# Kernel optimization log

Hardware: AMD Instinct MI355X
Metric: run time of the kernel (lower is better)

## Reference

```python
import jax, jax.numpy as jnp
import numpy as np

N_QUBITS = 15
N_LAYERS = 1
DIM = 2 ** N_QUBITS
N_PQC = 4 * N_QUBITS * N_LAYERS
CDTYPE = jnp.complex64


def _apply_1q(state, U, w):
    # state: (2,)*N tensor; apply 2x2 U on axis w
    s = jnp.tensordot(U, state, axes=((1,), (w,)))
    return jnp.moveaxis(s, 0, w)


def _ry_mat(theta):
    c = jnp.cos(theta / 2).astype(CDTYPE)
    s = jnp.sin(theta / 2).astype(CDTYPE)
    return jnp.stack([jnp.stack([c, -s]), jnp.stack([s, c])])


def _rx_mat(theta):
    c = jnp.cos(theta / 2).astype(CDTYPE)
    s = (-1j * jnp.sin(theta / 2)).astype(CDTYPE)
    return jnp.stack([jnp.stack([c, s]), jnp.stack([s, c])])


def _apply_crx(state, theta, ctrl, tgt):
    # controlled-RX: apply RX to target slice where control qubit = 1
    s0 = jax.lax.index_in_dim(state, 0, axis=ctrl, keepdims=False)
    s1 = jax.lax.index_in_dim(state, 1, axis=ctrl, keepdims=False)
    t = tgt if tgt < ctrl else tgt - 1
    s1 = _apply_1q(s1, _rx_mat(theta), t)
    return jnp.stack([s0, s1], axis=ctrl)


def _evolve(params, state):
    # ansatz 14 (Sim et al. 2019); params: [4*N_QUBITS*N_LAYERS]
    n = N_QUBITS
    idx = 0
    for _ in range(N_LAYERS):
        for i in range(n):
            state = _apply_1q(state, _ry_mat(params[idx]), i); idx += 1
        for i in range(n - 1, -1, -1):
            state = _apply_crx(state, params[idx], i, (i + 1) % n); idx += 1
        for i in range(n):
            state = _apply_1q(state, _ry_mat(params[idx]), i); idx += 1
        for i in [n - 1] + list(range(n - 1)):
            state = _apply_crx(state, params[idx], i, (i - 1) % n); idx += 1
    return state


def _measure_xyz(state):
    # expval of PauliX, PauliY, PauliZ on each wire -> [3*N_QUBITS] real
    xs, ys, zs = [], [], []
    for w in range(N_QUBITS):
        a = jnp.moveaxis(state, w, 0).reshape(2, -1)
        z01 = jnp.conj(a[0]) * a[1]
        xs.append(2.0 * jnp.sum(z01.real))
        ys.append(2.0 * jnp.sum(z01.imag))
        zs.append(jnp.sum(jnp.abs(a[0]) ** 2 - jnp.abs(a[1]) ** 2))
    return jnp.stack(xs + ys + zs)


def _forward(tokens_emb, W, b, qsvt_coeffs, lcu_coeffs_ri, ff_params):
    angles = tokens_emb @ W.T + b  # [L, N_PQC]
    lcu = lcu_coeffs_ri[:, 0] + 1j * lcu_coeffs_ri[:, 1]
    lcu = (lcu / jnp.maximum(jnp.sum(jnp.abs(lcu)), 1e-8)).astype(CDTYPE)
    e0 = jnp.zeros((DIM,), CDTYPE).at[0].set(1.0)

    def apply_lcu(mono):
        norm = jnp.linalg.norm(mono)
        small = norm < 1e-8
        safe = jnp.where(small, 1.0, norm)
        init = jnp.where(small, e0, mono / safe).reshape((2,) * N_QUBITS)
        evolved = jax.vmap(lambda p: _evolve(p, init).reshape(-1))(angles)  # [L, DIM]
        out = jnp.einsum('td,t->d', evolved, lcu)
        return jnp.where(small, 1.0, norm) * out

    acc = qsvt_coeffs[0] * e0
    mono = e0
    for k in range(1, qsvt_coeffs.shape[0]):
        mono = apply_lcu(mono)
        acc = acc + qsvt_coeffs[k] * mono
    acc = acc / jnp.maximum(jnp.sum(jnp.abs(qsvt_coeffs)), 1e-8)
    snorm = jnp.linalg.norm(acc)
    small = snorm < 1e-8
    safe = jnp.where(small, 1.0, snorm)
    ff_in = jnp.where(small, e0, acc / safe).reshape((2,) * N_QUBITS)
    final = _evolve(ff_params, ff_in)
    return _measure_xyz(final)


def setup_inputs() -> dict:
    key = jax.random.key(0)
    ks = jax.random.split(key, 6)
    d_model, n_tokens = 1024, 32
    tokens_emb = jax.random.normal(ks[0], (n_tokens, d_model), jnp.float32)
    W = jax.random.normal(ks[1], (N_PQC, d_model), jnp.float32) / np.float32(np.sqrt(d_model))
    b = jax.random.normal(ks[2], (N_PQC,), jnp.float32) * 0.01
    qsvt_coeffs = jax.random.normal(ks[3], (4,), jnp.float32) * 0.1
    lcu_coeffs_ri = jax.random.normal(ks[4], (n_tokens, 2), jnp.float32)
    ff_params = jax.random.normal(ks[5], (N_PQC,), jnp.float32)
    return {"tokens_emb": tokens_emb, "W": W, "b": b, "qsvt_coeffs": qsvt_coeffs,
            "lcu_coeffs_ri": lcu_coeffs_ri, "ff_params": ff_params}


def reference(tokens_emb, W, b, qsvt_coeffs, lcu_coeffs_ri, ff_params):
    return _forward(tokens_emb, W, b, qsvt_coeffs, lcu_coeffs_ri, ff_params)
```

## Files before the change

kernel.cpp:

```cpp
#include <hip/hip_runtime.h>

#define NQ    15
#define DIM   32768
#define NTOK  32
#define NPQC  60
#define TPB   512
#define KREG  64
#define CHUNK 16

template<int... Is> struct iseq {};
template<int N, int... Is> struct mkseq : mkseq<N-1, N-1, Is...> {};
template<int... Is> struct mkseq<0, Is...> { using type = iseq<Is...>; };

__device__ __forceinline__ float wsum(float v){
  #pragma unroll
  for (int m = 1; m < 64; m <<= 1) v += __shfl_xor(v, m, 64);
  return v;
}


template<int CPOS>
__device__ __forceinline__ bool cbit(int r, int tid, int blk){
  if constexpr (CPOS < 0)        return true;
  else if constexpr (CPOS == 0)  return (r & 1) != 0;
  else if constexpr (CPOS == 10) return (r & 2) != 0;
  else if constexpr (CPOS == 11) return (r & 4) != 0;
  else if constexpr (CPOS <= 9)  return ((tid >> (CPOS - 1)) & 1) != 0;
  else                           return ((blk >> (CPOS - 12)) & 1) != 0;
}

template<int TPOS, int CPOS, bool RX>
__device__ __forceinline__ void gate_rl(float2 cs, float (&vr)[8], float (&vi)[8], int tid, int blk){
  constexpr int tm = (TPOS == 0) ? 1 : (TPOS == 10 ? 2 : 4);
  const float c = cs.x, s = cs.y;
  #pragma unroll
  for (int r0 = 0; r0 < 8; ++r0){
    if (r0 & tm) continue;
    const int r1 = r0 | tm;
    const bool act = cbit<CPOS>(r0, tid, blk);
    const float ar = vr[r0], ai = vi[r0], br = vr[r1], bi = vi[r1];
    if (act){
      if constexpr (RX){
        vr[r0] = fmaf(c, ar,  s * bi); vi[r0] = fmaf(c, ai, -s * br);
        vr[r1] = fmaf(c, br,  s * ai); vi[r1] = fmaf(c, bi, -s * ar);
      } else {
        vr[r0] = fmaf(c, ar, -s * br); vi[r0] = fmaf(c, ai, -s * bi);
        vr[r1] = fmaf(c, br,  s * ar); vi[r1] = fmaf(c, bi,  s * ai);
      }
    }
  }
}

template<int TPOS, int CPOS, bool RX>
__device__ __forceinline__ void gate_ln(float2 cs, float (&vr)[8], float (&vi)[8], int tid, int blk){
  constexpr int bm = 1 << (TPOS - 1);
  const float c = cs.x, s = cs.y;
  const int side = (tid >> (TPOS - 1)) & 1;
  const float sg = side ? s : -s;
  #pragma unroll
  for (int r = 0; r < 8; ++r){
    const float pr = __shfl_xor(vr[r], bm, 64);
    const float pi = __shfl_xor(vi[r], bm, 64);
    const bool act = cbit<CPOS>(r, tid, blk);
    float nr, ni;
    if constexpr (RX){ nr = fmaf(c, vr[r],  s * pi); ni = fmaf(c, vi[r], -s * pr); }
    else             { nr = fmaf(c, vr[r], sg * pr); ni = fmaf(c, vi[r], sg * pi); }
    if (act){ vr[r] = nr; vi[r] = ni; }
  }
}

template<int TPOS, int CPOS, bool RX>
__device__ __forceinline__ void gate_wv(float2 cs, float (&vr)[8], float (&vi)[8], int tid, int blk, float2* ex){
  constexpr int tb = TPOS - 1;
  const int ptid = tid ^ (1 << tb);
  const float c = cs.x, s = cs.y;
  const int side = (tid >> tb) & 1;
  const float sg = side ? s : -s;
  __syncthreads();
  #pragma unroll
  for (int r = 0; r < 8; ++r) ex[(r << 9) | tid] = make_float2(vr[r], vi[r]);
  __syncthreads();
  #pragma unroll
  for (int r = 0; r < 8; ++r){
    const float2 p = ex[(r << 9) | ptid];
    const bool act = cbit<CPOS>(r, tid, blk);
    float nr, ni;
    if constexpr (RX){ nr = fmaf(c, vr[r],  s * p.y); ni = fmaf(c, vi[r], -s * p.x); }
    else             { nr = fmaf(c, vr[r], sg * p.x); ni = fmaf(c, vi[r], sg * p.y); }
    if (act){ vr[r] = nr; vi[r] = ni; }
  }
}

template<int TPOS, int CPOS, bool RX>
__device__ __forceinline__ void G(float2 cs, float (&vr)[8], float (&vi)[8], int tid, int blk, float2* ex){
  if constexpr (TPOS == 0 || TPOS == 10 || TPOS == 11) gate_rl<TPOS,CPOS,RX>(cs, vr, vi, tid, blk);
  else if constexpr (TPOS <= 6)                        gate_ln<TPOS,CPOS,RX>(cs, vr, vi, tid, blk);
  else                                                 gate_wv<TPOS,CPOS,RX>(cs, vr, vi, tid, blk, ex);
}

#define SEG_LOAD(SRC)                                                        \
  {                                                                          \
    const int t2 = tid << 1;                                                 \
    _Pragma("unroll")                                                        \
    for (int rh = 0; rh < 4; ++rh){                                          \
      const int r2 = rh >> 1, r1 = rh & 1, ra = (r1 << 1) | (r2 << 2);       \
      const float4 v = *reinterpret_cast<const float4*>(&(SRC)[(r2 << 11) + (r1 << 10) + t2]); \
      vr[ra] = v.x; vi[ra] = v.y; vr[ra + 1] = v.z; vi[ra + 1] = v.w;        \
    }                                                                        \
  }

__global__ __launch_bounds__(512) void seg1_k(const float2* __restrict__ in, float2* __restrict__ out,
    const float2* __restrict__ cs, int csStride, const float* __restrict__ parts, int np,
    int finalMode, const float* __restrict__ qsvt)
{
  __shared__ float2 ex[4096];
  __shared__ float2 gcs[12];
  const int tid = threadIdx.x, blk = blockIdx.x, tok = blockIdx.y;
  if (tid < 12) gcs[tid] = cs[tok * csStride + tid];
  bool small = false; float inv = 1.f;
  if (np > 0){
    const int lane = tid & 63;
    float p = lane < np ? parts[lane] : 0.f;
    const float nv = sqrtf(wsum(p));
    if (finalMode){
      const float qs = fmaxf(fabsf(qsvt[0]) + fabsf(qsvt[1]) + fabsf(qsvt[2]) + fabsf(qsvt[3]), 1e-8f);
      small = (nv / qs) < 1e-8f;
    } else small = nv < 1e-8f;
    inv = small ? 0.f : 1.f / nv;
  }
  float vr[8], vi[8];
  const float2* src = in + (blk << 12);
  {
    const int t2 = tid << 1;
    #pragma unroll
    for (int rh = 0; rh < 4; ++rh){
      const int r2 = rh >> 1, r1 = rh & 1, ra = (r1 << 1) | (r2 << 2);
      const float4 v = *reinterpret_cast<const float4*>(&src[(r2 << 11) + (r1 << 10) + t2]);
      vr[ra] = v.x * inv; vi[ra] = v.y * inv; vr[ra + 1] = v.z * inv; vi[ra + 1] = v.w * inv;
    }
  }
  if (small){
    #pragma unroll
    for (int r = 0; r < 8; ++r){ vr[r] = (blk == 0 && tid == 0 && r == 0) ? 1.f : 0.f; vi[r] = 0.f; }
  }
  __syncthreads();
  G<11,-1,false>(gcs[0], vr, vi, tid, blk, ex);
  G<10,-1,false>(gcs[1], vr, vi, tid, blk, ex);
  G< 9,-1,false>(gcs[2], vr, vi, tid, blk, ex);
  G< 8,-1,false>(gcs[3], vr, vi, tid, blk, ex);
  G< 7,-1,false>(gcs[4], vr, vi, tid, blk, ex);
  G< 6,-1,false>(gcs[5], vr, vi, tid, blk, ex);
  G< 5,-1,false>(gcs[6], vr, vi, tid, blk, ex);
  G< 4,-1,false>(gcs[7], vr, vi, tid, blk, ex);
  G< 3,-1,false>(gcs[8], vr, vi, tid, blk, ex);
  G< 2,-1,false>(gcs[9], vr, vi, tid, blk, ex);
  G< 1,-1,false>(gcs[10], vr, vi, tid, blk, ex);
  G< 0,-1,false>(gcs[11], vr, vi, tid, blk, ex);
  float2* dst = out + ((size_t)tok << 15);
  const int bb = ((blk & 1) << 5) | ((blk & 2) << 5) | ((blk & 4) << 8);
  const int tb = ((tid & 15) << 1) | ((tid & 112) << 3) | ((tid & 384) << 5);
  #pragma unroll
  for (int r1 = 0; r1 < 2; ++r1)
    #pragma unroll
    for (int r0 = 0; r0 < 2; ++r0){
      const int r = r0 | (r1 << 1);
      const int a = bb + tb + (r0 << 11) + (r1 << 14);
      *reinterpret_cast<float4*>(&dst[a]) = make_float4(vr[r], vi[r], vr[r + 4], vi[r + 4]);
    }
}

__global__ __launch_bounds__(512) void seg2_k(const float2* __restrict__ in, float2* __restrict__ out,
    const float2* __restrict__ cs, int csStride)
{
  __shared__ float2 ex[4096];
  __shared__ float2 gcs[15];
  const int tid = threadIdx.x, blk = blockIdx.x, tok = blockIdx.y;
  if (tid < 15) gcs[tid] = cs[tok * csStride + 12 + tid];
  float vr[8], vi[8];
  const float2* src = in + ((size_t)tok << 15) + (blk << 12);
  SEG_LOAD(src);
  __syncthreads();
  G<10,-1,false>(gcs[0], vr, vi, tid, blk, ex);
  G< 6,-1,false>(gcs[1], vr, vi, tid, blk, ex);
  G< 5,-1,false>(gcs[2], vr, vi, tid, blk, ex);
  G< 0, 5,true >(gcs[3], vr, vi, tid, blk, ex);
  G< 5, 6,true >(gcs[4], vr, vi, tid, blk, ex);
  G< 6,10,true >(gcs[5], vr, vi, tid, blk, ex);
  G<10,11,true >(gcs[6], vr, vi, tid, blk, ex);
  G<11, 1,true >(gcs[7], vr, vi, tid, blk, ex);
  G< 1, 2,true >(gcs[8], vr, vi, tid, blk, ex);
  G< 2, 3,true >(gcs[9], vr, vi, tid, blk, ex);
  G< 3, 4,true >(gcs[10], vr, vi, tid, blk, ex);
  G< 4, 7,true >(gcs[11], vr, vi, tid, blk, ex);
  G< 7, 8,true >(gcs[12], vr, vi, tid, blk, ex);
  G< 8, 9,true >(gcs[13], vr, vi, tid, blk, ex);
  G< 9,12,true >(gcs[14], vr, vi, tid, blk, ex);
  float2* dst = out + ((size_t)tok << 15);
  const int bb = ((blk & 1) << 11) | ((blk & 2) << 5) | ((blk & 4) << 3);
  const int tb = ((tid & 7) << 1) | ((tid & 8) << 7) | ((tid & 16) << 8) | ((tid & 32) << 8) | ((tid & 448) << 1);
  #pragma unroll
  for (int r1 = 0; r1 < 2; ++r1)
    #pragma unroll
    for (int r0 = 0; r0 < 2; ++r0){
      const int r = r0 | (r1 << 1);
      const int a = bb + tb + (r0 << 4) + (r1 << 14);
      *reinterpret_cast<float4*>(&dst[a]) = make_float4(vr[r], vi[r], vr[r + 4], vi[r + 4]);
    }
}

__global__ __launch_bounds__(512) void seg3_k(const float2* __restrict__ in, float2* __restrict__ out,
    const float2* __restrict__ cs, int csStride)
{
  __shared__ float2 ex[4096];
  __shared__ float2 gcs[15];
  const int tid = threadIdx.x, blk = blockIdx.x, tok = blockIdx.y;
  if (tid < 15) gcs[tid] = cs[tok * csStride + 27 + tid];
  float vr[8], vi[8];
  const float2* src = in + ((size_t)tok << 15) + (blk << 12);
  SEG_LOAD(src);
  __syncthreads();
  G<11, 6,true >(gcs[0], vr, vi, tid, blk, ex);
  G< 6, 5,true >(gcs[1], vr, vi, tid, blk, ex);
  G< 5, 4,true >(gcs[2], vr, vi, tid, blk, ex);
  G< 4,-1,false>(gcs[3], vr, vi, tid, blk, ex);
  G< 5,-1,false>(gcs[4], vr, vi, tid, blk, ex);
  G< 6,-1,false>(gcs[5], vr, vi, tid, blk, ex);
  G<11,-1,false>(gcs[6], vr, vi, tid, blk, ex);
  G< 9,-1,false>(gcs[7], vr, vi, tid, blk, ex);
  G< 8,-1,false>(gcs[8], vr, vi, tid, blk, ex);
  G< 7,-1,false>(gcs[9], vr, vi, tid, blk, ex);
  G<10,-1,false>(gcs[10], vr, vi, tid, blk, ex);
  G< 3,-1,false>(gcs[11], vr, vi, tid, blk, ex);
  G< 2,-1,false>(gcs[12], vr, vi, tid, blk, ex);
  G< 1,-1,false>(gcs[13], vr, vi, tid, blk, ex);
  G< 0,-1,false>(gcs[14], vr, vi, tid, blk, ex);
  float2* dst = out + ((size_t)tok << 15);
  const int bb = ((blk & 1) << 5) | ((blk & 2) << 5) | ((blk & 4) << 8);
  const int tb = ((tid & 1) << 13) | ((tid & 2) << 13) | ((tid & 60) >> 1) | ((tid & 448) << 1);
  #pragma unroll
  for (int r2 = 0; r2 < 2; ++r2)
    #pragma unroll
    for (int r0 = 0; r0 < 2; ++r0){
      const int r = r0 | (r2 << 2);
      const int a = bb + tb + (r0 << 12) + (r2 << 11);
      *reinterpret_cast<float4*>(&dst[a]) = make_float4(vr[r], vi[r], vr[r + 2], vi[r + 2]);
    }
}

__global__ __launch_bounds__(512) void seg4_k(const float2* __restrict__ in, float2* __restrict__ out,
    const float2* __restrict__ cs, int csStride)
{
  __shared__ float2 ex[4096];
  __shared__ float2 gcs[14];
  const int tid = threadIdx.x, blk = blockIdx.x, tok = blockIdx.y;
  if (tid < 14) gcs[tid] = cs[tok * csStride + 42 + tid];
  float vr[8], vi[8];
  const float2* src = in + ((size_t)tok << 15) + (blk << 12);
  SEG_LOAD(src);
  __syncthreads();
  G<10,-1,false>(gcs[0], vr, vi, tid, blk, ex);
  G< 6,-1,false>(gcs[1], vr, vi, tid, blk, ex);
  G< 5,-1,false>(gcs[2], vr, vi, tid, blk, ex);
  G< 6, 5,true >(gcs[3], vr, vi, tid, blk, ex);
  G< 5, 2,true >(gcs[4], vr, vi, tid, blk, ex);
  G< 2, 3,true >(gcs[5], vr, vi, tid, blk, ex);
  G< 3, 4,true >(gcs[6], vr, vi, tid, blk, ex);
  G< 4,11,true >(gcs[7], vr, vi, tid, blk, ex);
  G<11, 9,true >(gcs[8], vr, vi, tid, blk, ex);
  G< 9, 8,true >(gcs[9], vr, vi, tid, blk, ex);
  G< 8, 7,true >(gcs[10], vr, vi, tid, blk, ex);
  G< 7, 0,true >(gcs[11], vr, vi, tid, blk, ex);
  G< 0, 1,true >(gcs[12], vr, vi, tid, blk, ex);
  G< 1,14,true >(gcs[13], vr, vi, tid, blk, ex);
  float2* dst = out + ((size_t)tok << 15);
  const int bb = ((blk & 1) << 10) | ((blk & 2) << 2) | ((blk & 4) << 2);
  const int tb = ((tid & 1) << 5) | ((tid & 2) << 13) | ((tid & 4) << 11) | ((tid & 8) << 9)
               | ((tid & 48) >> 3) | ((tid & 448) << 1);
  #pragma unroll
  for (int r2 = 0; r2 < 2; ++r2)
    #pragma unroll
    for (int r0 = 0; r0 < 2; ++r0){
      const int r = r0 | (r2 << 2);
      const int a = bb + tb + (r0 << 6) + (r2 << 11);
      *reinterpret_cast<float4*>(&dst[a]) = make_float4(vr[r], vi[r], vr[r + 2], vi[r + 2]);
    }
}

__global__ __launch_bounds__(512) void seg5_k(const float2* __restrict__ in, float2* __restrict__ out,
    const float2* __restrict__ cs, int csStride)
{
  __shared__ float2 ex[4096];
  __shared__ float2 gcs[4];
  const int tid = threadIdx.x, blk = blockIdx.x, tok = blockIdx.y;
  if (tid < 4) gcs[tid] = cs[tok * csStride + 56 + tid];
  float vr[8], vi[8];
  const float2* src = in + ((size_t)tok << 15) + (blk << 12);
  SEG_LOAD(src);
  __syncthreads();
  G< 4, 3,true >(gcs[0], vr, vi, tid, blk, ex);
  G< 3,10,true >(gcs[1], vr, vi, tid, blk, ex);
  G<10, 0,true >(gcs[2], vr, vi, tid, blk, ex);
  G< 0, 2,true >(gcs[3], vr, vi, tid, blk, ex);
  float2* dst = out + ((size_t)tok << 15);
  const int bb = blk << 9;
  const int tb = ((tid & 1) << 12) | ((tid & 2) << 12) | ((tid & 508) >> 1);
  #pragma unroll
  for (int r2 = 0; r2 < 2; ++r2)
    #pragma unroll
    for (int r0 = 0; r0 < 2; ++r0){
      const int r = r0 | (r2 << 2);
      const int a = bb + tb + (r0 << 14) + (r2 << 8);
      *reinterpret_cast<float4*>(&dst[a]) = make_float4(vr[r], vi[r], vr[r + 2], vi[r + 2]);
    }
}

__global__ void angles2_kernel(const float* __restrict__ emb, const float* __restrict__ W,
                               const float* __restrict__ b, float2* __restrict__ csarr)
{
  const int p = blockIdx.x, t = blockIdx.y, lane = threadIdx.x;
  const float* er = emb + (size_t)t * 1024;
  const float* wr = W + (size_t)p * 1024;
  float s = 0.f;
  for (int i = lane; i < 1024; i += 64) s = fmaf(er[i], wr[i], s);
  s = wsum(s);
  if (lane == 0){
    const float a = (s + b[p]) * 0.5f;
    csarr[t * NPQC + p] = make_float2(cosf(a), sinf(a));
  }
}

__global__ void prep_kernel(const float* __restrict__ ri, float2* __restrict__ lcu,
                            const float* __restrict__ ffp, float2* __restrict__ csf)
{
  const int t = threadIdx.x;
  float re = 0.f, im = 0.f, mag = 0.f;
  if (t < NTOK){ re = ri[2 * t]; im = ri[2 * t + 1]; mag = sqrtf(re * re + im * im); }
  const float ssum = wsum(mag);
  const float denom = fmaxf(ssum, 1e-8f);
  if (t < NTOK) lcu[t] = make_float2(re / denom, im / denom);
  if (t < NPQC){ const float a = ffp[t] * 0.5f; csf[t] = make_float2(cosf(a), sinf(a)); }
}

__global__ void init2_kernel(float2* __restrict__ monoA, float2* __restrict__ acc,
                             const float* __restrict__ qsvt)
{
  const int d = (blockIdx.x << 9) | threadIdx.x;
  monoA[d] = make_float2(d == 0 ? 1.f : 0.f, 0.f);
  acc[d]   = make_float2(d == 0 ? qsvt[0] : 0.f, 0.f);
}

__global__ __launch_bounds__(512) void combine2_k(const float2* __restrict__ ev, const float2* __restrict__ lcu,
    const float* __restrict__ partsPrev, int np, const float* __restrict__ qsvt, int k,
    float2* __restrict__ mono_out, float2* __restrict__ acc,
    float* __restrict__ pM, float* __restrict__ pA)
{
  __shared__ float red[16];
  const int tid = threadIdx.x;
  const int d = (blockIdx.x << 9) | tid;
  float scale = 1.f;
  if (np > 0){
    const int lane = tid & 63;
    float p = lane < np ? partsPrev[lane] : 0.f;
    const float nv = sqrtf(wsum(p));
    scale = (nv < 1e-8f) ? 1.f : nv;
  }
  float sr = 0.f, si = 0.f;
  #pragma unroll
  for (int t = 0; t < NTOK; ++t){
    const float2 e = ev[((size_t)t << 15) + d];
    const float2 c = lcu[t];
    sr += e.x * c.x - e.y * c.y;
    si += e.x * c.y + e.y * c.x;
  }
  sr *= scale; si *= scale;
  mono_out[d] = make_float2(sr, si);
  const float q = qsvt[k];
  float2 a = acc[d];
  a = make_float2(fmaf(q, sr, a.x), fmaf(q, si, a.y));
  acc[d] = a;
  float m2 = fmaf(sr, sr, si * si);
  float a2 = fmaf(a.x, a.x, a.y * a.y);
  m2 = wsum(m2); a2 = wsum(a2);
  const int lane = tid & 63, wv = tid >> 6;
  if (lane == 0){ red[wv] = m2; red[8 + wv] = a2; }
  __syncthreads();
  if (tid == 0){
    float t1 = 0.f, t2 = 0.f;
    for (int i = 0; i < 8; ++i){ t1 += red[i]; t2 += red[8 + i]; }
    pM[blockIdx.x] = t1; pA[blockIdx.x] = t2;
  }
}

__global__ void measure_l1(const float2* __restrict__ st, float* __restrict__ out)
{
  __shared__ float rx[16], ryy[16], rz[16];
  const int tid = threadIdx.x;
  const int lane = tid & 63, wv = tid >> 6;
  const int abit[15] = {11,10,9,8,7,6,5,4,3,2,1,0,14,13,12};
  for (int w = 0; w < NQ; ++w){
    const int ab = abit[w];
    const int m = 1 << ab;
    float x = 0.f, y = 0.f, z = 0.f;
    for (int d = tid; d < DIM / 2; d += 1024){
      const int i0 = ((d >> ab) << (ab + 1)) | (d & (m - 1));
      const float2 a0 = st[i0];
      const float2 a1 = st[i0 | m];
      x += a0.x * a1.x + a0.y * a1.y;
      y += a0.x * a1.y - a0.y * a1.x;
      z += (a0.x * a0.x + a0.y * a0.y) - (a1.x * a1.x + a1.y * a1.y);
    }
    x = wsum(x); y = wsum(y); z = wsum(z);
    if (lane == 0){ rx[wv] = x; ryy[wv] = y; rz[wv] = z; }
    __syncthreads();
    if (tid == 0){
      float sx = 0.f, sy = 0.f, sz = 0.f;
      for (int i = 0; i < 16; ++i){ sx += rx[i]; sy += ryy[i]; sz += rz[i]; }
      out[w] = 2.0f * sx; out[NQ + w] = 2.0f * sy; out[2 * NQ + w] = sz;
    }
    __syncthreads();
  }
}


constexpr int crx1_fb(int j){ return j == 0 ? 14 : j - 1; }
constexpr int crx1_cb(int j){ return j; }
constexpr int crx2_fb(int k){ return k == 0 ? 1 : (k == 1 ? 0 : 16 - k); }
constexpr int crx2_cb(int k){ return k == 0 ? 0 : (k == 1 ? 14 : 15 - k); }

template<int FB, int CB, bool RX>
__device__ __forceinline__ void gate(float c, float s,
    float (&vr)[KREG], float (&vi)[KREG], const int tid,
    float* __restrict__ lr, float* __restrict__ li)
{
  if constexpr (FB < 6) {
    constexpr int m = 1 << FB;
    #pragma unroll
    for (int r0 = 0; r0 < KREG; ++r0) {
      if ((r0 & m) != 0) continue;
      const int r1 = r0 | m;
      bool a;
      if constexpr (CB < 0)      a = true;
      else if constexpr (CB < 6) a = ((r0 >> CB) & 1) != 0;
      else                       a = ((tid >> (CB - 6)) & 1) != 0;
      if (a) {
        if constexpr (RX) {
          float n0r = fmaf(c, vr[r0],  s * vi[r1]);
          float n0i = fmaf(c, vi[r0], -s * vr[r1]);
          float n1r = fmaf(c, vr[r1],  s * vi[r0]);
          float n1i = fmaf(c, vi[r1], -s * vr[r0]);
          vr[r0] = n0r; vi[r0] = n0i; vr[r1] = n1r; vi[r1] = n1i;
        } else {
          float n0r = fmaf(c, vr[r0], -s * vr[r1]);
          float n0i = fmaf(c, vi[r0], -s * vi[r1]);
          float n1r = fmaf(c, vr[r1],  s * vr[r0]);
          float n1i = fmaf(c, vi[r1],  s * vi[r0]);
          vr[r0] = n0r; vi[r0] = n0i; vr[r1] = n1r; vi[r1] = n1i;
        }
      }
    }
  } else if constexpr (FB < 12) {
    constexpr int bm = 1 << (FB - 6);
    const int side = (tid >> (FB - 6)) & 1;
    const float sg = side ? s : -s;
    #pragma unroll
    for (int r = 0; r < KREG; ++r) {
      float pr = __shfl_xor(vr[r], bm, 64);
      float pi = __shfl_xor(vi[r], bm, 64);
      bool a;
      if constexpr (CB < 0)      a = true;
      else if constexpr (CB < 6) a = ((r >> CB) & 1) != 0;
      else                       a = ((tid >> (CB - 6)) & 1) != 0;
      float nr, ni;
      if constexpr (RX) { nr = fmaf(c, vr[r],  s * pi); ni = fmaf(c, vi[r], -s * pr); }
      else              { nr = fmaf(c, vr[r], sg * pr); ni = fmaf(c, vi[r], sg * pi); }
      if (a) { vr[r] = nr; vi[r] = ni; }
    }
  } else {
    constexpr int bm = 1 << (FB - 6);
    const int side = (tid >> (FB - 6)) & 1;
    const float sg = side ? s : -s;
    const int ptid = tid ^ bm;
    #pragma unroll
    for (int ch = 0; ch < KREG / CHUNK; ++ch) {
      __syncthreads();
      #pragma unroll
      for (int j = 0; j < CHUNK; ++j) {
        lr[j * TPB + tid] = vr[ch * CHUNK + j];
        li[j * TPB + tid] = vi[ch * CHUNK + j];
      }
      __syncthreads();
      #pragma unroll
      for (int j = 0; j < CHUNK; ++j) {
        const int r = ch * CHUNK + j;
        float pr = lr[j * TPB + ptid];
        float pi = li[j * TPB + ptid];
        bool a;
        if constexpr (CB < 0)      a = true;
        else if constexpr (CB < 6) a = ((r >> CB) & 1) != 0;
        else                       a = ((tid >> (CB - 6)) & 1) != 0;
        float nr, ni;
        if constexpr (RX) { nr = fmaf(c, vr[r],  s * pi); ni = fmaf(c, vi[r], -s * pr); }
        else              { nr = fmaf(c, vr[r], sg * pr); ni = fmaf(c, vi[r], sg * pi); }
        if (a) { vr[r] = nr; vi[r] = ni; }
      }
    }
  }
}

template<int... Is>
__device__ __forceinline__ void evolve_seq(iseq<Is...>,
    float (&vr)[KREG], float (&vi)[KREG], int tid,
    float* __restrict__ lr, float* __restrict__ li,
    const float* __restrict__ csh, const float* __restrict__ snh)
{
  (gate<14 - Is, -1, false>(csh[Is], snh[Is], vr, vi, tid, lr, li), ...);
  (gate<crx1_fb(Is), crx1_cb(Is), true>(csh[15 + Is], snh[15 + Is], vr, vi, tid, lr, li), ...);
  (gate<14 - Is, -1, false>(csh[30 + Is], snh[30 + Is], vr, vi, tid, lr, li), ...);
  (gate<crx2_fb(Is), crx2_cb(Is), true>(csh[45 + Is], snh[45 + Is], vr, vi, tid, lr, li), ...);
}

__global__ __launch_bounds__(TPB, 2) void evolve_kernel(
    const float* __restrict__ angles, int astride,
    const float2* __restrict__ in_state,
    const float* __restrict__ norms, int slot, int mode,
    const float2* __restrict__ lcu,
    float2* __restrict__ out)
{
  __shared__ float lr[CHUNK * TPB];
  __shared__ float li[CHUNK * TPB];
  __shared__ float csh[NPQC], snh[NPQC];
  const int tid = threadIdx.x;
  {
    const float* ang = angles + (size_t)blockIdx.x * astride;
    if (tid < NPQC) {
      float a = ang[tid] * 0.5f;
      csh[tid] = cosf(a);
      snh[tid] = sinf(a);
    }
  }
  const float nv = norms[slot];
  bool small;
  if (mode == 1) {
    float qs = fmaxf(norms[4], 1e-8f);
    small = (nv / qs) < 1e-8f;
  } else {
    small = nv < 1e-8f;
  }
  const float inv = small ? 0.0f : 1.0f / nv;
  float vr[KREG], vi[KREG];
  const int base = tid * KREG;
  #pragma unroll
  for (int r = 0; r < KREG; ++r) {
    float2 v = in_state[base + r];
    vr[r] = small ? ((base + r) == 0 ? 1.0f : 0.0f) : v.x * inv;
    vi[r] = small ? 0.0f : v.y * inv;
  }
  __syncthreads();
  evolve_seq(typename mkseq<NQ>::type{}, vr, vi, tid, lr, li, csh, snh);
  if (mode == 0) {
    float2* o = out + (size_t)blockIdx.x * DIM;
    #pragma unroll
    for (int r = 0; r < KREG; ++r) o[base + r] = make_float2(vr[r], vi[r]);
  } else if (mode == 1) {
    #pragma unroll
    for (int r = 0; r < KREG; ++r) out[base + r] = make_float2(vr[r], vi[r]);
  } else {
    const float2 w = lcu[blockIdx.x];
    #pragma unroll
    for (int r = 0; r < KREG; ++r) {
      float xr = w.x * vr[r] - w.y * vi[r];
      float xi = w.x * vi[r] + w.y * vr[r];
      atomicAdd(&out[base + r].x, xr);
      atomicAdd(&out[base + r].y, xi);
    }
  }
}

__global__ void angles_kernel(const float* __restrict__ emb, const float* __restrict__ W,
                              const float* __restrict__ b, float* __restrict__ angles)
{
  const int p = blockIdx.x, t = blockIdx.y, lane = threadIdx.x;
  const float* er = emb + (size_t)t * 1024;
  const float* wr = W + (size_t)p * 1024;
  float s = 0.f;
  for (int i = lane; i < 1024; i += 64) s = fmaf(er[i], wr[i], s);
  s = wsum(s);
  if (lane == 0) angles[t * NPQC + p] = s + b[p];
}

__global__ void lcu_kernel(const float* __restrict__ ri, float2* __restrict__ lcu)
{
  const int t = threadIdx.x;
  float re = 0.f, im = 0.f, mag = 0.f;
  if (t < NTOK) { re = ri[2 * t]; im = ri[2 * t + 1]; mag = sqrtf(re * re + im * im); }
  float ssum = wsum(mag);
  float denom = fmaxf(ssum, 1e-8f);
  if (t < NTOK) lcu[t] = make_float2(re / denom, im / denom);
}

__global__ void init_kernel(float2* __restrict__ monoA, float2* __restrict__ monoB,
                            float2* __restrict__ acc, const float* __restrict__ qsvt,
                            float* __restrict__ norms)
{
  const int d = blockIdx.x * blockDim.x + threadIdx.x;
  if (d < DIM) {
    monoA[d] = make_float2(d == 0 ? 1.f : 0.f, 0.f);
    monoB[d] = make_float2(0.f, 0.f);
    acc[d]   = make_float2(d == 0 ? qsvt[0] : 0.f, 0.f);
  }
  if (d == 0)
    norms[4] = fabsf(qsvt[0]) + fabsf(qsvt[1]) + fabsf(qsvt[2]) + fabsf(qsvt[3]);
}

__global__ void norm_kernel(const float2* __restrict__ v, float* __restrict__ norms, int slot)
{
  __shared__ float red[16];
  const int tid = threadIdx.x;
  float s = 0.f;
  for (int d = tid; d < DIM; d += 1024) {
    float2 a = v[d];
    s = fmaf(a.x, a.x, fmaf(a.y, a.y, s));
  }
  s = wsum(s);
  const int lane = tid & 63, wv = tid >> 6;
  if (lane == 0) red[wv] = s;
  __syncthreads();
  if (tid == 0) {
    float t = 0.f;
    for (int i = 0; i < 16; ++i) t += red[i];
    norms[slot] = sqrtf(t);
  }
}

__global__ void combine_kernel(const float2* __restrict__ evolved,
                               const float2* __restrict__ lcu,
                               const float* __restrict__ norms, int slot,
                               const float* __restrict__ qsvt, int k,
                               float2* __restrict__ mono_out,
                               float2* __restrict__ acc)
{
  const int d = blockIdx.x * blockDim.x + threadIdx.x;
  const float nvv = norms[slot];
  const float scale = (nvv < 1e-8f) ? 1.0f : nvv;
  float sr = 0.f, si = 0.f;
  #pragma unroll
  for (int t = 0; t < NTOK; ++t) {
    float2 e = evolved[(size_t)t * DIM + d];
    float2 c = lcu[t];
    sr += e.x * c.x - e.y * c.y;
    si += e.x * c.y + e.y * c.x;
  }
  sr *= scale; si *= scale;
  mono_out[d] = make_float2(sr, si);
  const float q = qsvt[k];
  float2 a = acc[d];
  acc[d] = make_float2(fmaf(q, sr, a.x), fmaf(q, si, a.y));
}

__global__ void finish_kernel(float2* __restrict__ mono2, float2* __restrict__ acc,
                              float2* __restrict__ zero_buf,
                              const float* __restrict__ norms, int slot,
                              const float* __restrict__ qsvt, int k)
{
  const int d = blockIdx.x * blockDim.x + threadIdx.x;
  const float nvv = norms[slot];
  const float scale = (nvv < 1e-8f) ? 1.0f : nvv;
  float2 v = mono2[d];
  v.x *= scale; v.y *= scale;
  mono2[d] = v;
  const float q = qsvt[k];
  float2 a = acc[d];
  acc[d] = make_float2(fmaf(q, v.x, a.x), fmaf(q, v.y, a.y));
  zero_buf[d] = make_float2(0.f, 0.f);
}

__global__ void measure_kernel(const float2* __restrict__ st, float* __restrict__ out)
{
  __shared__ float rx[16], ryy[16], rz[16];
  const int tid = threadIdx.x;
  const int lane = tid & 63, wv = tid >> 6;
  for (int w = 0; w < NQ; ++w) {
    const int fb = 14 - w;
    const int m = 1 << fb;
    float x = 0.f, y = 0.f, z = 0.f;
    for (int d = tid; d < DIM / 2; d += 1024) {
      int i0 = ((d >> fb) << (fb + 1)) | (d & (m - 1));
      float2 a0 = st[i0];
      float2 a1 = st[i0 | m];
      x += a0.x * a1.x + a0.y * a1.y;
      y += a0.x * a1.y - a0.y * a1.x;
      z += (a0.x * a0.x + a0.y * a0.y) - (a1.x * a1.x + a1.y * a1.y);
    }
    x = wsum(x); y = wsum(y); z = wsum(z);
    if (lane == 0) { rx[wv] = x; ryy[wv] = y; rz[wv] = z; }
    __syncthreads();
    if (tid == 0) {
      float sx = 0.f, sy = 0.f, sz = 0.f;
      for (int i = 0; i < 16; ++i) { sx += rx[i]; sy += ryy[i]; sz += rz[i]; }
      out[w] = 2.0f * sx; out[NQ + w] = 2.0f * sy; out[2 * NQ + w] = sz;
    }
    __syncthreads();
  }
}


extern "C" void kernel_launch(void* const* d_in, const int* in_sizes, int n_in,
                              void* d_out, int out_size, void* d_ws, size_t ws_size,
                              hipStream_t stream)
{
  const float* emb   = (const float*)d_in[0];
  const float* W     = (const float*)d_in[1];
  const float* b     = (const float*)d_in[2];
  const float* qsvt  = (const float*)d_in[3];
  const float* lcuri = (const float*)d_in[4];
  const float* ffp   = (const float*)d_in[5];
  float* out = (float*)d_out;

  char* ws = (char*)d_ws;
  size_t off = 0;
  auto nxt = [&](size_t bytes) { size_t o = off; off = (off + bytes + 255) & ~(size_t)255; return o; };

  const size_t o_cs   = nxt((size_t)NTOK * NPQC * sizeof(float2));
  const size_t o_csf  = nxt(NPQC * sizeof(float2));
  const size_t o_lcu2 = nxt(NTOK * sizeof(float2));
  const size_t o_pm   = nxt(3 * 64 * sizeof(float));
  const size_t o_pa   = nxt(64 * sizeof(float));
  const size_t o_mA2  = nxt((size_t)DIM * sizeof(float2));
  const size_t o_mB2  = nxt((size_t)DIM * sizeof(float2));
  const size_t o_acc2 = nxt((size_t)DIM * sizeof(float2));
  const size_t o_fin2 = nxt((size_t)DIM * sizeof(float2));
  const size_t o_bufA = nxt((size_t)NTOK * DIM * sizeof(float2));
  const size_t o_bufB = nxt((size_t)NTOK * DIM * sizeof(float2));
  const size_t newNeed = off;

  if (ws_size >= newNeed) {
    float2* csarr = (float2*)(ws + o_cs);
    float2* csf   = (float2*)(ws + o_csf);
    float2* lcu   = (float2*)(ws + o_lcu2);
    float*  pMbuf = (float*)(ws + o_pm);
    float*  pA    = (float*)(ws + o_pa);
    float2* monoA = (float2*)(ws + o_mA2);
    float2* monoB = (float2*)(ws + o_mB2);
    float2* acc   = (float2*)(ws + o_acc2);
    float2* fin   = (float2*)(ws + o_fin2);
    float2* bufA  = (float2*)(ws + o_bufA);
    float2* bufB  = (float2*)(ws + o_bufB);

    angles2_kernel<<<dim3(NPQC, NTOK), 64, 0, stream>>>(emb, W, b, csarr);
    prep_kernel<<<1, 64, 0, stream>>>(lcuri, lcu, ffp, csf);
    init2_kernel<<<64, 512, 0, stream>>>(monoA, acc, qsvt);

    float2* mIn = monoA;
    float2* mOut = monoB;
    const float* prevPM = nullptr;
    for (int k = 1; k <= 3; ++k) {
      const int np = prevPM ? 64 : 0;
      seg1_k<<<dim3(8, NTOK), 512, 0, stream>>>(mIn, bufA, csarr, NPQC, prevPM, np, 0, qsvt);
      seg2_k<<<dim3(8, NTOK), 512, 0, stream>>>(bufA, bufB, csarr, NPQC);
      seg3_k<<<dim3(8, NTOK), 512, 0, stream>>>(bufB, bufA, csarr, NPQC);
      seg4_k<<<dim3(8, NTOK), 512, 0, stream>>>(bufA, bufB, csarr, NPQC);
      seg5_k<<<dim3(8, NTOK), 512, 0, stream>>>(bufB, bufA, csarr, NPQC);
      float* pMk = pMbuf + (size_t)(k - 1) * 64;
      combine2_k<<<64, 512, 0, stream>>>(bufA, lcu, prevPM, np, qsvt, k, mOut, acc, pMk, pA);
      prevPM = pMk;
      float2* tmp = mIn; mIn = mOut; mOut = tmp;
    }

    seg1_k<<<dim3(8, 1), 512, 0, stream>>>(acc, bufA, csf, 0, pA, 64, 1, qsvt);
    seg2_k<<<dim3(8, 1), 512, 0, stream>>>(bufA, bufB, csf, 0);
    seg3_k<<<dim3(8, 1), 512, 0, stream>>>(bufB, bufA, csf, 0);
    seg4_k<<<dim3(8, 1), 512, 0, stream>>>(bufA, bufB, csf, 0);
    seg5_k<<<dim3(8, 1), 512, 0, stream>>>(bufB, fin, csf, 0);
    measure_l1<<<1, 1024, 0, stream>>>(fin, out);
    return;
  }

  off = 0;
  const size_t o_ang = nxt(NTOK * NPQC * sizeof(float));
  const size_t o_lcu = nxt(NTOK * sizeof(float2));
  const size_t o_nrm = nxt(16 * sizeof(float));
  const size_t o_mA  = nxt((size_t)DIM * sizeof(float2));
  const size_t o_mB  = nxt((size_t)DIM * sizeof(float2));
  const size_t o_acc = nxt((size_t)DIM * sizeof(float2));
  const size_t o_fin = nxt((size_t)DIM * sizeof(float2));
  const size_t o_ev  = nxt((size_t)NTOK * DIM * sizeof(float2));
  const bool bigws = ws_size >= off;

  float*  angles  = (float*)(ws + o_ang);
  float2* lcu     = (float2*)(ws + o_lcu);
  float*  norms   = (float*)(ws + o_nrm);
  float2* monoA   = (float2*)(ws + o_mA);
  float2* monoB   = (float2*)(ws + o_mB);
  float2* acc     = (float2*)(ws + o_acc);
  float2* fin     = (float2*)(ws + o_fin);
  float2* evolved = (float2*)(ws + o_ev);

  angles_kernel<<<dim3(NPQC, NTOK), 64, 0, stream>>>(emb, W, b, angles);
  lcu_kernel<<<1, 64, 0, stream>>>(lcuri, lcu);
  init_kernel<<<DIM / 256, 256, 0, stream>>>(monoA, monoB, acc, qsvt, norms);

  float2* mono = monoA;
  float2* mono2 = monoB;
  for (int k = 1; k <= 3; ++k) {
    norm_kernel<<<1, 1024, 0, stream>>>(mono, norms, k - 1);
    if (bigws) {
      evolve_kernel<<<NTOK, TPB, 0, stream>>>(angles, NPQC, mono, norms, k - 1, 0, lcu, evolved);
      combine_kernel<<<DIM / 256, 256, 0, stream>>>(evolved, lcu, norms, k - 1, qsvt, k, mono2, acc);
    } else {
      evolve_kernel<<<NTOK, TPB, 0, stream>>>(angles, NPQC, mono, norms, k - 1, 2, lcu, mono2);
      finish_kernel<<<DIM / 256, 256, 0, stream>>>(mono2, acc, mono, norms, k - 1, qsvt, k);
    }
    float2* tmp = mono; mono = mono2; mono2 = tmp;
  }

  norm_kernel<<<1, 1024, 0, stream>>>(acc, norms, 3);
  evolve_kernel<<<1, TPB, 0, stream>>>(ffp, 0, acc, norms, 3, 1, lcu, fin);
  measure_kernel<<<1, 1024, 0, stream>>>(fin, out);
}
```

Before: 334.0 us.

## Fuse segment kernels into one persistent kernel with atomic grid barriers

```diff
diff --git a/kernel.cpp b/kernel.cpp
--- a/kernel.cpp
+++ b/kernel.cpp
@@ -4,13 +4,6 @@
 #define DIM   32768
 #define NTOK  32
 #define NPQC  60
-#define TPB   512
-#define KREG  64
-#define CHUNK 16
-
-template<int... Is> struct iseq {};
-template<int N, int... Is> struct mkseq : mkseq<N-1, N-1, Is...> {};
-template<int... Is> struct mkseq<0, Is...> { using type = iseq<Is...>; };
 
 __device__ __forceinline__ float wsum(float v){
   #pragma unroll
@@ -109,14 +102,12 @@
     }                                                                        \
   }
 
-__global__ __launch_bounds__(512) void seg1_k(const float2* __restrict__ in, float2* __restrict__ out,
-    const float2* __restrict__ cs, int csStride, const float* __restrict__ parts, int np,
-    int finalMode, const float* __restrict__ qsvt)
-{
-  __shared__ float2 ex[4096];
-  __shared__ float2 gcs[12];
-  const int tid = threadIdx.x, blk = blockIdx.x, tok = blockIdx.y;
-  if (tid < 12) gcs[tid] = cs[tok * csStride + tid];
+
+__device__ __forceinline__ void d_seg1(const float2* __restrict__ mono, float2* __restrict__ outTok,
+    const float2* __restrict__ cs, const float* __restrict__ parts, int np, int finalMode,
+    const float* __restrict__ qsvt, int tid, int blk, float2* ex, float2* gcs)
+{
+  if (tid < 12) gcs[tid] = cs[tid];
   bool small = false; float inv = 1.f;
   if (np > 0){
     const int lane = tid & 63;
@@ -129,7 +120,7 @@
     inv = small ? 0.f : 1.f / nv;
   }
   float vr[8], vi[8];
-  const float2* src = in + (blk << 12);
+  const float2* src = mono + (blk << 12);
   {
     const int t2 = tid << 1;
     #pragma unroll
@@ -156,7 +147,7 @@
   G< 2,-1,false>(gcs[9], vr, vi, tid, blk, ex);
   G< 1,-1,false>(gcs[10], vr, vi, tid, blk, ex);
   G< 0,-1,false>(gcs[11], vr, vi, tid, blk, ex);
-  float2* dst = out + ((size_t)tok << 15);
+  float2* dst = outTok;
   const int bb = ((blk & 1) << 5) | ((blk & 2) << 5) | ((blk & 4) << 8);
   const int tb = ((tid & 15) << 1) | ((tid & 112) << 3) | ((tid & 384) << 5);
   #pragma unroll
@@ -169,15 +160,12 @@
     }
 }
 
-__global__ __launch_bounds__(512) void seg2_k(const float2* __restrict__ in, float2* __restrict__ out,
-    const float2* __restrict__ cs, int csStride)
-{
-  __shared__ float2 ex[4096];
-  __shared__ float2 gcs[15];
-  const int tid = threadIdx.x, blk = blockIdx.x, tok = blockIdx.y;
-  if (tid < 15) gcs[tid] = cs[tok * csStride + 12 + tid];
+__device__ __forceinline__ void d_seg2(const float2* __restrict__ inTok, float2* __restrict__ outTok,
+    const float2* __restrict__ cs, int tid, int blk, float2* ex, float2* gcs)
+{
+  if (tid < 15) gcs[tid] = cs[12 + tid];
   float vr[8], vi[8];
-  const float2* src = in + ((size_t)tok << 15) + (blk << 12);
+  const float2* src = inTok + (blk << 12);
   SEG_LOAD(src);
   __syncthreads();
   G<10,-1,false>(gcs[0], vr, vi, tid, blk, ex);
@@ -195,7 +183,7 @@
   G< 7, 8,true >(gcs[12], vr, vi, tid, blk, ex);
   G< 8, 9,true >(gcs[13], vr, vi, tid, blk, ex);
   G< 9,12,true >(gcs[14], vr, vi, tid, blk, ex);
-  float2* dst = out + ((size_t)tok << 15);
+  float2* dst = outTok;
   const int bb = ((blk & 1) << 11) | ((blk & 2) << 5) | ((blk & 4) << 3);
   const int tb = ((tid & 7) << 1) | ((tid & 8) << 7) | ((tid & 16) << 8) | ((tid & 32) << 8) | ((tid & 448) << 1);
   #pragma unroll
@@ -208,15 +196,12 @@
     }
 }
 
-__global__ __launch_bounds__(512) void seg3_k(const float2* __restrict__ in, float2* __restrict__ out,
-    const float2* __restrict__ cs, int csStride)
-{
-  __shared__ float2 ex[4096];
-  __shared__ float2 gcs[15];
-  const int tid = threadIdx.x, blk = blockIdx.x, tok = blockIdx.y;
-  if (tid < 15) gcs[tid] = cs[tok * csStride + 27 + tid];
+__device__ __forceinline__ void d_seg3(const float2* __restrict__ inTok, float2* __restrict__ outTok,
+    const float2* __restrict__ cs, int tid, int blk, float2* ex, float2* gcs)
+{
+  if (tid < 15) gcs[tid] = cs[27 + tid];
   float vr[8], vi[8];
-  const float2* src = in + ((size_t)tok << 15) + (blk << 12);
+  const float2* src = inTok + (blk << 12);
   SEG_LOAD(src);
   __syncthreads();
   G<11, 6,true >(gcs[0], vr, vi, tid, blk, ex);
@@ -234,7 +219,7 @@
   G< 2,-1,false>(gcs[12], vr, vi, tid, blk, ex);
   G< 1,-1,false>(gcs[13], vr, vi, tid, blk, ex);
   G< 0,-1,false>(gcs[14], vr, vi, tid, blk, ex);
-  float2* dst = out + ((size_t)tok << 15);
+  float2* dst = outTok;
   const int bb = ((blk & 1) << 5) | ((blk & 2) << 5) | ((blk & 4) << 8);
   const int tb = ((tid & 1) << 13) | ((tid & 2) << 13) | ((tid & 60) >> 1) | ((tid & 448) << 1);
   #pragma unroll
@@ -247,15 +232,12 @@
     }
 }
 
-__global__ __launch_bounds__(512) void seg4_k(const float2* __restrict__ in, float2* __restrict__ out,
-    const float2* __restrict__ cs, int csStride)
-{
-  __shared__ float2 ex[4096];
-  __shared__ float2 gcs[14];
-  const int tid = threadIdx.x, blk = blockIdx.x, tok = blockIdx.y;
-  if (tid < 14) gcs[tid] = cs[tok * csStride + 42 + tid];
+__device__ __forceinline__ void d_seg4(const float2* __restrict__ inTok, float2* __restrict__ outTok,
+    const float2* __restrict__ cs, int tid, int blk, float2* ex, float2* gcs)
+{
+  if (tid < 14) gcs[tid] = cs[42 + tid];
   float vr[8], vi[8];
-  const float2* src = in + ((size_t)tok << 15) + (blk << 12);
+  const float2* src = inTok + (blk << 12);
   SEG_LOAD(src);
   __syncthreads();
   G<10,-1,false>(gcs[0], vr, vi, tid, blk, ex);
@@ -272,7 +254,7 @@
   G< 7, 0,true >(gcs[11], vr, vi, tid, blk, ex);
   G< 0, 1,true >(gcs[12], vr, vi, tid, blk, ex);
   G< 1,14,true >(gcs[13], vr, vi, tid, blk, ex);
-  float2* dst = out + ((size_t)tok << 15);
+  float2* dst = outTok;
   const int bb = ((blk & 1) << 10) | ((blk & 2) << 2) | ((blk & 4) << 2);
   const int tb = ((tid & 1) << 5) | ((tid & 2) << 13) | ((tid & 4) << 11) | ((tid & 8) << 9)
                | ((tid & 48) >> 3) | ((tid & 448) << 1);
@@ -286,22 +268,19 @@
     }
 }
 
-__global__ __launch_bounds__(512) void seg5_k(const float2* __restrict__ in, float2* __restrict__ out,
-    const float2* __restrict__ cs, int csStride)
-{
-  __shared__ float2 ex[4096];
-  __shared__ float2 gcs[4];
-  const int tid = threadIdx.x, blk = blockIdx.x, tok = blockIdx.y;
-  if (tid < 4) gcs[tid] = cs[tok * csStride + 56 + tid];
+__device__ __forceinline__ void d_seg5(const float2* __restrict__ inTok, float2* __restrict__ outTok,
+    const float2* __restrict__ cs, int tid, int blk, float2* ex, float2* gcs)
+{
+  if (tid < 4) gcs[tid] = cs[56 + tid];
   float vr[8], vi[8];
-  const float2* src = in + ((size_t)tok << 15) + (blk << 12);
+  const float2* src = inTok + (blk << 12);
   SEG_LOAD(src);
   __syncthreads();
   G< 4, 3,true >(gcs[0], vr, vi, tid, blk, ex);
   G< 3,10,true >(gcs[1], vr, vi, tid, blk, ex);
   G<10, 0,true >(gcs[2], vr, vi, tid, blk, ex);
   G< 0, 2,true >(gcs[3], vr, vi, tid, blk, ex);
-  float2* dst = out + ((size_t)tok << 15);
+  float2* dst = outTok;
   const int bb = blk << 9;
   const int tb = ((tid & 1) << 12) | ((tid & 2) << 12) | ((tid & 508) >> 1);
   #pragma unroll
@@ -314,49 +293,12 @@
     }
 }
 
-__global__ void angles2_kernel(const float* __restrict__ emb, const float* __restrict__ W,
-                               const float* __restrict__ b, float2* __restrict__ csarr)
-{
-  const int p = blockIdx.x, t = blockIdx.y, lane = threadIdx.x;
-  const float* er = emb + (size_t)t * 1024;
-  const float* wr = W + (size_t)p * 1024;
-  float s = 0.f;
-  for (int i = lane; i < 1024; i += 64) s = fmaf(er[i], wr[i], s);
-  s = wsum(s);
-  if (lane == 0){
-    const float a = (s + b[p]) * 0.5f;
-    csarr[t * NPQC + p] = make_float2(cosf(a), sinf(a));
-  }
-}
-
-__global__ void prep_kernel(const float* __restrict__ ri, float2* __restrict__ lcu,
-                            const float* __restrict__ ffp, float2* __restrict__ csf)
-{
-  const int t = threadIdx.x;
-  float re = 0.f, im = 0.f, mag = 0.f;
-  if (t < NTOK){ re = ri[2 * t]; im = ri[2 * t + 1]; mag = sqrtf(re * re + im * im); }
-  const float ssum = wsum(mag);
-  const float denom = fmaxf(ssum, 1e-8f);
-  if (t < NTOK) lcu[t] = make_float2(re / denom, im / denom);
-  if (t < NPQC){ const float a = ffp[t] * 0.5f; csf[t] = make_float2(cosf(a), sinf(a)); }
-}
-
-__global__ void init2_kernel(float2* __restrict__ monoA, float2* __restrict__ acc,
-                             const float* __restrict__ qsvt)
-{
-  const int d = (blockIdx.x << 9) | threadIdx.x;
-  monoA[d] = make_float2(d == 0 ? 1.f : 0.f, 0.f);
-  acc[d]   = make_float2(d == 0 ? qsvt[0] : 0.f, 0.f);
-}
-
-__global__ __launch_bounds__(512) void combine2_k(const float2* __restrict__ ev, const float2* __restrict__ lcu,
+__device__ __forceinline__ void d_combine(const float2* __restrict__ ev, const float2* __restrict__ lcu,
     const float* __restrict__ partsPrev, int np, const float* __restrict__ qsvt, int k,
     float2* __restrict__ mono_out, float2* __restrict__ acc,
-    float* __restrict__ pM, float* __restrict__ pA)
-{
-  __shared__ float red[16];
-  const int tid = threadIdx.x;
-  const int d = (blockIdx.x << 9) | tid;
+    float* __restrict__ pMo, float* __restrict__ pAo, int bid, int tid, float* red)
+{
+  const int d = (bid << 9) | tid;
   float scale = 1.f;
   if (np > 0){
     const int lane = tid & 63;
@@ -387,8 +329,159 @@
   if (tid == 0){
     float t1 = 0.f, t2 = 0.f;
     for (int i = 0; i < 8; ++i){ t1 += red[i]; t2 += red[8 + i]; }
-    pM[blockIdx.x] = t1; pA[blockIdx.x] = t2;
-  }
+    pMo[bid] = t1; pAo[bid] = t2;
+  }
+}
+
+__device__ __forceinline__ void bar_arrive_wait(unsigned* cnt, unsigned target){
+  __syncthreads();
+  if (threadIdx.x == 0){
+    __threadfence();
+    atomicAdd(cnt, 1u);
+    while (atomicAdd(cnt, 0u) < target) __builtin_amdgcn_s_sleep(4);
+    __threadfence();
+  }
+  __syncthreads();
+}
+
+__global__ __launch_bounds__(512) void mega_k(
+    const float2* __restrict__ csarr, const float2* __restrict__ csf,
+    const float2* __restrict__ lcu, const float* __restrict__ qsvt,
+    float2* monoA, float2* monoB, float2* acc, float2* fin,
+    float2* bufA, float2* bufB,
+    float* pM, float* pA, float* partials, float* out,
+    unsigned* tcnt, unsigned* gcnt)
+{
+  __shared__ float2 ex[4096];
+  __shared__ float2 gcs[16];
+  __shared__ float red[16];
+  __shared__ float sredx[8][16], sredy[8][16], sredz[8][16];
+  const int tid = threadIdx.x;
+  const int bid = blockIdx.x;
+  const int blk = bid & 7, tok = bid >> 3;
+  int tgen = 0, ggen = 0;
+  float2* const bA = bufA + ((size_t)tok << 15);
+  float2* const bB = bufB + ((size_t)tok << 15);
+  const float2* const csTok = csarr + tok * NPQC;
+
+  #pragma unroll 1
+  for (int r = 0; r < 3; ++r){
+    const float2* min_ = (r & 1) ? monoB : monoA;
+    float2* mout       = (r & 1) ? monoA : monoB;
+    const float* prevPM = (r == 0) ? (const float*)nullptr : (pM + (size_t)(r - 1) * 64);
+    const int np = (r == 0) ? 0 : 64;
+    d_seg1(min_, bA, csTok, prevPM, np, 0, qsvt, tid, blk, ex, gcs);
+    bar_arrive_wait(tcnt + tok, 8u * (unsigned)(++tgen));
+    d_seg2(bA, bB, csTok, tid, blk, ex, gcs);
+    bar_arrive_wait(tcnt + tok, 8u * (unsigned)(++tgen));
+    d_seg3(bB, bA, csTok, tid, blk, ex, gcs);
+    bar_arrive_wait(tcnt + tok, 8u * (unsigned)(++tgen));
+    d_seg4(bA, bB, csTok, tid, blk, ex, gcs);
+    bar_arrive_wait(tcnt + tok, 8u * (unsigned)(++tgen));
+    d_seg5(bB, bA, csTok, tid, blk, ex, gcs);
+    bar_arrive_wait(gcnt, 256u * (unsigned)(++ggen));
+    if (bid < 64)
+      d_combine(bufA, lcu, prevPM, np, qsvt, r + 1, mout, acc, pM + (size_t)r * 64, pA, bid, tid, red);
+    bar_arrive_wait(gcnt, 256u * (unsigned)(++ggen));
+  }
+
+  if (tok == 0){
+    d_seg1(acc, bufA, csf, pA, 64, 1, qsvt, tid, blk, ex, gcs);
+    bar_arrive_wait(tcnt + tok, 8u * (unsigned)(++tgen));
+    d_seg2(bufA, bufB, csf, tid, blk, ex, gcs);
+    bar_arrive_wait(tcnt + tok, 8u * (unsigned)(++tgen));
+    d_seg3(bufB, bufA, csf, tid, blk, ex, gcs);
+    bar_arrive_wait(tcnt + tok, 8u * (unsigned)(++tgen));
+    d_seg4(bufA, bufB, csf, tid, blk, ex, gcs);
+    bar_arrive_wait(tcnt + tok, 8u * (unsigned)(++tgen));
+    d_seg5(bufB, fin, csf, tid, blk, ex, gcs);
+  }
+  bar_arrive_wait(gcnt, 256u * (unsigned)(++ggen));
+
+  if (bid < 64){
+    const int g = (bid << 9) | tid;
+    const float2 a = fin[g];
+    ex[tid] = a;
+    __syncthreads();
+    const int lane = tid & 63, wv = tid >> 6;
+    const int abit[15] = {11,10,9,8,7,6,5,4,3,2,1,0,14,13,12};
+    #pragma unroll
+    for (int w = 0; w < 15; ++w){
+      const int ab = abit[w];
+      const int m = 1 << ab;
+      float2 p;
+      if (ab < 6){ p.x = __shfl_xor(a.x, m, 64); p.y = __shfl_xor(a.y, m, 64); }
+      else if (ab < 9){ p = ex[tid ^ m]; }
+      else { p = fin[g ^ m]; }
+      const bool lower = (g & m) == 0;
+      float x = lower ? (a.x * p.x + a.y * p.y) : 0.f;
+      float y = lower ? (a.x * p.y - a.y * p.x) : 0.f;
+      float z = (lower ? 1.f : -1.f) * (a.x * a.x + a.y * a.y);
+      x = wsum(x); y = wsum(y); z = wsum(z);
+      if (lane == 0){ sredx[wv][w] = x; sredy[wv][w] = y; sredz[wv][w] = z; }
+    }
+    __syncthreads();
+    if (tid < 45){
+      const int plane = tid / 15, w = tid % 15;
+      float s = 0.f;
+      #pragma unroll
+      for (int i = 0; i < 8; ++i)
+        s += (plane == 0) ? sredx[i][w] : (plane == 1) ? sredy[i][w] : sredz[i][w];
+      partials[bid * 45 + tid] = (plane < 2 ? 2.f : 1.f) * s;
+    }
+  }
+  bar_arrive_wait(gcnt, 256u * (unsigned)(++ggen));
+  if (bid == 0 && tid < 45){
+    float s = 0.f;
+    for (int i = 0; i < 64; ++i) s += partials[i * 45 + tid];
+    out[tid] = s;
+  }
+}
+
+
+__global__ __launch_bounds__(512) void seg1_k(const float2* __restrict__ in, float2* __restrict__ out,
+    const float2* __restrict__ cs, int csStride, const float* __restrict__ parts, int np,
+    int finalMode, const float* __restrict__ qsvt)
+{
+  __shared__ float2 ex[4096]; __shared__ float2 gcs[16];
+  d_seg1(in, out + ((size_t)blockIdx.y << 15), cs + blockIdx.y * csStride, parts, np, finalMode, qsvt,
+         threadIdx.x, blockIdx.x, ex, gcs);
+}
+__global__ __launch_bounds__(512) void seg2_k(const float2* __restrict__ in, float2* __restrict__ out,
+    const float2* __restrict__ cs, int csStride)
+{
+  __shared__ float2 ex[4096]; __shared__ float2 gcs[16];
+  d_seg2(in + ((size_t)blockIdx.y << 15), out + ((size_t)blockIdx.y << 15), cs + blockIdx.y * csStride,
+         threadIdx.x, blockIdx.x, ex, gcs);
+}
+__global__ __launch_bounds__(512) void seg3_k(const float2* __restrict__ in, float2* __restrict__ out,
+    const float2* __restrict__ cs, int csStride)
+{
+  __shared__ float2 ex[4096]; __shared__ float2 gcs[16];
+  d_seg3(in + ((size_t)blockIdx.y << 15), out + ((size_t)blockIdx.y << 15), cs + blockIdx.y * csStride,
+         threadIdx.x, blockIdx.x, ex, gcs);
+}
+__global__ __launch_bounds__(512) void seg4_k(const float2* __restrict__ in, float2* __restrict__ out,
+    const float2* __restrict__ cs, int csStride)
+{
+  __shared__ float2 ex[4096]; __shared__ float2 gcs[16];
+  d_seg4(in + ((size_t)blockIdx.y << 15), out + ((size_t)blockIdx.y << 15), cs + blockIdx.y * csStride,
+         threadIdx.x, blockIdx.x, ex, gcs);
+}
+__global__ __launch_bounds__(512) void seg5_k(const float2* __restrict__ in, float2* __restrict__ out,
+    const float2* __restrict__ cs, int csStride)
+{
+  __shared__ float2 ex[4096]; __shared__ float2 gcs[16];
+  d_seg5(in + ((size_t)blockIdx.y << 15), out + ((size_t)blockIdx.y << 15), cs + blockIdx.y * csStride,
+         threadIdx.x, blockIdx.x, ex, gcs);
+}
+__global__ __launch_bounds__(512) void combine2_k(const float2* __restrict__ ev, const float2* __restrict__ lcu,
+    const float* __restrict__ partsPrev, int np, const float* __restrict__ qsvt, int k,
+    float2* __restrict__ mono_out, float2* __restrict__ acc,
+    float* __restrict__ pM, float* __restrict__ pA)
+{
+  __shared__ float red[16];
+  d_combine(ev, lcu, partsPrev, np, qsvt, k, mono_out, acc, pM, pA, blockIdx.x, threadIdx.x, red);
 }
 
 __global__ void measure_l1(const float2* __restrict__ st, float* __restrict__ out)
@@ -422,162 +515,8 @@
 }
 
 
-constexpr int crx1_fb(int j){ return j == 0 ? 14 : j - 1; }
-constexpr int crx1_cb(int j){ return j; }
-constexpr int crx2_fb(int k){ return k == 0 ? 1 : (k == 1 ? 0 : 16 - k); }
-constexpr int crx2_cb(int k){ return k == 0 ? 0 : (k == 1 ? 14 : 15 - k); }
-
-template<int FB, int CB, bool RX>
-__device__ __forceinline__ void gate(float c, float s,
-    float (&vr)[KREG], float (&vi)[KREG], const int tid,
-    float* __restrict__ lr, float* __restrict__ li)
-{
-  if constexpr (FB < 6) {
-    constexpr int m = 1 << FB;
-    #pragma unroll
-    for (int r0 = 0; r0 < KREG; ++r0) {
-      if ((r0 & m) != 0) continue;
-      const int r1 = r0 | m;
-      bool a;
-      if constexpr (CB < 0)      a = true;
-      else if constexpr (CB < 6) a = ((r0 >> CB) & 1) != 0;
-      else                       a = ((tid >> (CB - 6)) & 1) != 0;
-      if (a) {
-        if constexpr (RX) {
-          float n0r = fmaf(c, vr[r0],  s * vi[r1]);
-          float n0i = fmaf(c, vi[r0], -s * vr[r1]);
-          float n1r = fmaf(c, vr[r1],  s * vi[r0]);
-          float n1i = fmaf(c, vi[r1], -s * vr[r0]);
-          vr[r0] = n0r; vi[r0] = n0i; vr[r1] = n1r; vi[r1] = n1i;
-        } else {
-          float n0r = fmaf(c, vr[r0], -s * vr[r1]);
-          float n0i = fmaf(c, vi[r0], -s * vi[r1]);
-          float n1r = fmaf(c, vr[r1],  s * vr[r0]);
-          float n1i = fmaf(c, vi[r1],  s * vi[r0]);
-          vr[r0] = n0r; vi[r0] = n0i; vr[r1] = n1r; vi[r1] = n1i;
-        }
-      }
-    }
-  } else if constexpr (FB < 12) {
-    constexpr int bm = 1 << (FB - 6);
-    const int side = (tid >> (FB - 6)) & 1;
-    const float sg = side ? s : -s;
-    #pragma unroll
-    for (int r = 0; r < KREG; ++r) {
-      float pr = __shfl_xor(vr[r], bm, 64);
-      float pi = __shfl_xor(vi[r], bm, 64);
-      bool a;
-      if constexpr (CB < 0)      a = true;
-      else if constexpr (CB < 6) a = ((r >> CB) & 1) != 0;
-      else                       a = ((tid >> (CB - 6)) & 1) != 0;
-      float nr, ni;
-      if constexpr (RX) { nr = fmaf(c, vr[r],  s * pi); ni = fmaf(c, vi[r], -s * pr); }
-      else              { nr = fmaf(c, vr[r], sg * pr); ni = fmaf(c, vi[r], sg * pi); }
-      if (a) { vr[r] = nr; vi[r] = ni; }
-    }
-  } else {
-    constexpr int bm = 1 << (FB - 6);
-    const int side = (tid >> (FB - 6)) & 1;
-    const float sg = side ? s : -s;
-    const int ptid = tid ^ bm;
-    #pragma unroll
-    for (int ch = 0; ch < KREG / CHUNK; ++ch) {
-      __syncthreads();
-      #pragma unroll
-      for (int j = 0; j < CHUNK; ++j) {
-        lr[j * TPB + tid] = vr[ch * CHUNK + j];
-        li[j * TPB + tid] = vi[ch * CHUNK + j];
-      }
-      __syncthreads();
-      #pragma unroll
-      for (int j = 0; j < CHUNK; ++j) {
-        const int r = ch * CHUNK + j;
-        float pr = lr[j * TPB + ptid];
-        float pi = li[j * TPB + ptid];
-        bool a;
-        if constexpr (CB < 0)      a = true;
-        else if constexpr (CB < 6) a = ((r >> CB) & 1) != 0;
-        else                       a = ((tid >> (CB - 6)) & 1) != 0;
-        float nr, ni;
-        if constexpr (RX) { nr = fmaf(c, vr[r],  s * pi); ni = fmaf(c, vi[r], -s * pr); }
-        else              { nr = fmaf(c, vr[r], sg * pr); ni = fmaf(c, vi[r], sg * pi); }
-        if (a) { vr[r] = nr; vi[r] = ni; }
-      }
-    }
-  }
-}
-
-template<int... Is>
-__device__ __forceinline__ void evolve_seq(iseq<Is...>,
-    float (&vr)[KREG], float (&vi)[KREG], int tid,
-    float* __restrict__ lr, float* __restrict__ li,
-    const float* __restrict__ csh, const float* __restrict__ snh)
-{
-  (gate<14 - Is, -1, false>(csh[Is], snh[Is], vr, vi, tid, lr, li), ...);
-  (gate<crx1_fb(Is), crx1_cb(Is), true>(csh[15 + Is], snh[15 + Is], vr, vi, tid, lr, li), ...);
-  (gate<14 - Is, -1, false>(csh[30 + Is], snh[30 + Is], vr, vi, tid, lr, li), ...);
-  (gate<crx2_fb(Is), crx2_cb(Is), true>(csh[45 + Is], snh[45 + Is], vr, vi, tid, lr, li), ...);
-}
-
-__global__ __launch_bounds__(TPB, 2) void evolve_kernel(
-    const float* __restrict__ angles, int astride,
-    const float2* __restrict__ in_state,
-    const float* __restrict__ norms, int slot, int mode,
-    const float2* __restrict__ lcu,
-    float2* __restrict__ out)
-{
-  __shared__ float lr[CHUNK * TPB];
-  __shared__ float li[CHUNK * TPB];
-  __shared__ float csh[NPQC], snh[NPQC];
-  const int tid = threadIdx.x;
-  {
-    const float* ang = angles + (size_t)blockIdx.x * astride;
-    if (tid < NPQC) {
-      float a = ang[tid] * 0.5f;
-      csh[tid] = cosf(a);
-      snh[tid] = sinf(a);
-    }
-  }
-  const float nv = norms[slot];
-  bool small;
-  if (mode == 1) {
-    float qs = fmaxf(norms[4], 1e-8f);
-    small = (nv / qs) < 1e-8f;
-  } else {
-    small = nv < 1e-8f;
-  }
-  const float inv = small ? 0.0f : 1.0f / nv;
-  float vr[KREG], vi[KREG];
-  const int base = tid * KREG;
-  #pragma unroll
-  for (int r = 0; r < KREG; ++r) {
-    float2 v = in_state[base + r];
-    vr[r] = small ? ((base + r) == 0 ? 1.0f : 0.0f) : v.x * inv;
-    vi[r] = small ? 0.0f : v.y * inv;
-  }
-  __syncthreads();
-  evolve_seq(typename mkseq<NQ>::type{}, vr, vi, tid, lr, li, csh, snh);
-  if (mode == 0) {
-    float2* o = out + (size_t)blockIdx.x * DIM;
-    #pragma unroll
-    for (int r = 0; r < KREG; ++r) o[base + r] = make_float2(vr[r], vi[r]);
-  } else if (mode == 1) {
-    #pragma unroll
-    for (int r = 0; r < KREG; ++r) out[base + r] = make_float2(vr[r], vi[r]);
-  } else {
-    const float2 w = lcu[blockIdx.x];
-    #pragma unroll
-    for (int r = 0; r < KREG; ++r) {
-      float xr = w.x * vr[r] - w.y * vi[r];
-      float xi = w.x * vi[r] + w.y * vr[r];
-      atomicAdd(&out[base + r].x, xr);
-      atomicAdd(&out[base + r].y, xi);
-    }
-  }
-}
-
-__global__ void angles_kernel(const float* __restrict__ emb, const float* __restrict__ W,
-                              const float* __restrict__ b, float* __restrict__ angles)
+__global__ void angles2_kernel(const float* __restrict__ emb, const float* __restrict__ W,
+                               const float* __restrict__ b, float2* __restrict__ csarr)
 {
   const int p = blockIdx.x, t = blockIdx.y, lane = threadIdx.x;
   const float* er = emb + (size_t)t * 1024;
@@ -585,122 +524,31 @@
   float s = 0.f;
   for (int i = lane; i < 1024; i += 64) s = fmaf(er[i], wr[i], s);
   s = wsum(s);
-  if (lane == 0) angles[t * NPQC + p] = s + b[p];
-}
-
-__global__ void lcu_kernel(const float* __restrict__ ri, float2* __restrict__ lcu)
+  if (lane == 0){
+    const float a = (s + b[p]) * 0.5f;
+    csarr[t * NPQC + p] = make_float2(cosf(a), sinf(a));
+  }
+}
+
+__global__ void prep_kernel(const float* __restrict__ ri, float2* __restrict__ lcu,
+                            const float* __restrict__ ffp, float2* __restrict__ csf)
 {
   const int t = threadIdx.x;
   float re = 0.f, im = 0.f, mag = 0.f;
-  if (t < NTOK) { re = ri[2 * t]; im = ri[2 * t + 1]; mag = sqrtf(re * re + im * im); }
-  float ssum = wsum(mag);
-  float denom = fmaxf(ssum, 1e-8f);
+  if (t < NTOK){ re = ri[2 * t]; im = ri[2 * t + 1]; mag = sqrtf(re * re + im * im); }
+  const float ssum = wsum(mag);
+  const float denom = fmaxf(ssum, 1e-8f);
   if (t < NTOK) lcu[t] = make_float2(re / denom, im / denom);
-}
-
-__global__ void init_kernel(float2* __restrict__ monoA, float2* __restrict__ monoB,
-                            float2* __restrict__ acc, const float* __restrict__ qsvt,
-                            float* __restrict__ norms)
-{
-  const int d = blockIdx.x * blockDim.x + threadIdx.x;
-  if (d < DIM) {
-    monoA[d] = make_float2(d == 0 ? 1.f : 0.f, 0.f);
-    monoB[d] = make_float2(0.f, 0.f);
-    acc[d]   = make_float2(d == 0 ? qsvt[0] : 0.f, 0.f);
-  }
-  if (d == 0)
-    norms[4] = fabsf(qsvt[0]) + fabsf(qsvt[1]) + fabsf(qsvt[2]) + fabsf(qsvt[3]);
-}
-
-__global__ void norm_kernel(const float2* __restrict__ v, float* __restrict__ norms, int slot)
-{
-  __shared__ float red[16];
-  const int tid = threadIdx.x;
-  float s = 0.f;
-  for (int d = tid; d < DIM; d += 1024) {
-    float2 a = v[d];
-    s = fmaf(a.x, a.x, fmaf(a.y, a.y, s));
-  }
-  s = wsum(s);
-  const int lane = tid & 63, wv = tid >> 6;
-  if (lane == 0) red[wv] = s;
-  __syncthreads();
-  if (tid == 0) {
-    float t = 0.f;
-    for (int i = 0; i < 16; ++i) t += red[i];
-    norms[slot] = sqrtf(t);
-  }
-}
-
-__global__ void combine_kernel(const float2* __restrict__ evolved,
-                               const float2* __restrict__ lcu,
-                               const float* __restrict__ norms, int slot,
-                               const float* __restrict__ qsvt, int k,
-                               float2* __restrict__ mono_out,
-                               float2* __restrict__ acc)
-{
-  const int d = blockIdx.x * blockDim.x + threadIdx.x;
-  const float nvv = norms[slot];
-  const float scale = (nvv < 1e-8f) ? 1.0f : nvv;
-  float sr = 0.f, si = 0.f;
-  #pragma unroll
-  for (int t = 0; t < NTOK; ++t) {
-    float2 e = evolved[(size_t)t * DIM + d];
-    float2 c = lcu[t];
-    sr += e.x * c.x - e.y * c.y;
-    si += e.x * c.y + e.y * c.x;
-  }
-  sr *= scale; si *= scale;
-  mono_out[d] = make_float2(sr, si);
-  const float q = qsvt[k];
-  float2 a = acc[d];
-  acc[d] = make_float2(fmaf(q, sr, a.x), fmaf(q, si, a.y));
-}
-
-__global__ void finish_kernel(float2* __restrict__ mono2, float2* __restrict__ acc,
-                              float2* __restrict__ zero_buf,
-                              const float* __restrict__ norms, int slot,
-                              const float* __restrict__ qsvt, int k)
-{
-  const int d = blockIdx.x * blockDim.x + threadIdx.x;
-  const float nvv = norms[slot];
-  const float scale = (nvv < 1e-8f) ? 1.0f : nvv;
-  float2 v = mono2[d];
-  v.x *= scale; v.y *= scale;
-  mono2[d] = v;
-  const float q = qsvt[k];
-  float2 a = acc[d];
-  acc[d] = make_float2(fmaf(q, v.x, a.x), fmaf(q, v.y, a.y));
-  zero_buf[d] = make_float2(0.f, 0.f);
-}
-
-__global__ void measure_kernel(const float2* __restrict__ st, float* __restrict__ out)
-{
-  __shared__ float rx[16], ryy[16], rz[16];
-  const int tid = threadIdx.x;
-  const int lane = tid & 63, wv = tid >> 6;
-  for (int w = 0; w < NQ; ++w) {
-    const int fb = 14 - w;
-    const int m = 1 << fb;
-    float x = 0.f, y = 0.f, z = 0.f;
-    for (int d = tid; d < DIM / 2; d += 1024) {
-      int i0 = ((d >> fb) << (fb + 1)) | (d & (m - 1));
-      float2 a0 = st[i0];
-      float2 a1 = st[i0 | m];
-      x += a0.x * a1.x + a0.y * a1.y;
-      y += a0.x * a1.y - a0.y * a1.x;
-      z += (a0.x * a0.x + a0.y * a0.y) - (a1.x * a1.x + a1.y * a1.y);
-    }
-    x = wsum(x); y = wsum(y); z = wsum(z);
-    if (lane == 0) { rx[wv] = x; ryy[wv] = y; rz[wv] = z; }
-    __syncthreads();
-    if (tid == 0) {
-      float sx = 0.f, sy = 0.f, sz = 0.f;
-      for (int i = 0; i < 16; ++i) { sx += rx[i]; sy += ryy[i]; sz += rz[i]; }
-      out[w] = 2.0f * sx; out[NQ + w] = 2.0f * sy; out[2 * NQ + w] = sz;
-    }
-    __syncthreads();
-  }
+  if (t < NPQC){ const float a = ffp[t] * 0.5f; csf[t] = make_float2(cosf(a), sinf(a)); }
+}
+
+__global__ void init3_kernel(float2* __restrict__ monoA, float2* __restrict__ acc,
+                             const float* __restrict__ qsvt, unsigned* __restrict__ cnts)
+{
+  const int d = (blockIdx.x << 9) | threadIdx.x;
+  monoA[d] = make_float2(d == 0 ? 1.f : 0.f, 0.f);
+  acc[d]   = make_float2(d == 0 ? qsvt[0] : 0.f, 0.f);
+  if (d < 40) cnts[d] = 0u;
 }
 
 
@@ -725,95 +573,60 @@
   const size_t o_lcu2 = nxt(NTOK * sizeof(float2));
   const size_t o_pm   = nxt(3 * 64 * sizeof(float));
   const size_t o_pa   = nxt(64 * sizeof(float));
+  const size_t o_part = nxt(64 * 45 * sizeof(float));
+  const size_t o_cnt  = nxt(64 * sizeof(unsigned));
   const size_t o_mA2  = nxt((size_t)DIM * sizeof(float2));
   const size_t o_mB2  = nxt((size_t)DIM * sizeof(float2));
   const size_t o_acc2 = nxt((size_t)DIM * sizeof(float2));
   const size_t o_fin2 = nxt((size_t)DIM * sizeof(float2));
   const size_t o_bufA = nxt((size_t)NTOK * DIM * sizeof(float2));
   const size_t o_bufB = nxt((size_t)NTOK * DIM * sizeof(float2));
-  const size_t newNeed = off;
-
-  if (ws_size >= newNeed) {
-    float2* csarr = (float2*)(ws + o_cs);
-    float2* csf   = (float2*)(ws + o_csf);
-    float2* lcu   = (float2*)(ws + o_lcu2);
-    float*  pMbuf = (float*)(ws + o_pm);
-    float*  pA    = (float*)(ws + o_pa);
-    float2* monoA = (float2*)(ws + o_mA2);
-    float2* monoB = (float2*)(ws + o_mB2);
-    float2* acc   = (float2*)(ws + o_acc2);
-    float2* fin   = (float2*)(ws + o_fin2);
-    float2* bufA  = (float2*)(ws + o_bufA);
-    float2* bufB  = (float2*)(ws + o_bufB);
-
-    angles2_kernel<<<dim3(NPQC, NTOK), 64, 0, stream>>>(emb, W, b, csarr);
-    prep_kernel<<<1, 64, 0, stream>>>(lcuri, lcu, ffp, csf);
-    init2_kernel<<<64, 512, 0, stream>>>(monoA, acc, qsvt);
-
-    float2* mIn = monoA;
-    float2* mOut = monoB;
-    const float* prevPM = nullptr;
-    for (int k = 1; k <= 3; ++k) {
-      const int np = prevPM ? 64 : 0;
-      seg1_k<<<dim3(8, NTOK), 512, 0, stream>>>(mIn, bufA, csarr, NPQC, prevPM, np, 0, qsvt);
-      seg2_k<<<dim3(8, NTOK), 512, 0, stream>>>(bufA, bufB, csarr, NPQC);
-      seg3_k<<<dim3(8, NTOK), 512, 0, stream>>>(bufB, bufA, csarr, NPQC);
-      seg4_k<<<dim3(8, NTOK), 512, 0, stream>>>(bufA, bufB, csarr, NPQC);
-      seg5_k<<<dim3(8, NTOK), 512, 0, stream>>>(bufB, bufA, csarr, NPQC);
-      float* pMk = pMbuf + (size_t)(k - 1) * 64;
-      combine2_k<<<64, 512, 0, stream>>>(bufA, lcu, prevPM, np, qsvt, k, mOut, acc, pMk, pA);
-      prevPM = pMk;
-      float2* tmp = mIn; mIn = mOut; mOut = tmp;
-    }
-
-    seg1_k<<<dim3(8, 1), 512, 0, stream>>>(acc, bufA, csf, 0, pA, 64, 1, qsvt);
-    seg2_k<<<dim3(8, 1), 512, 0, stream>>>(bufA, bufB, csf, 0);
-    seg3_k<<<dim3(8, 1), 512, 0, stream>>>(bufB, bufA, csf, 0);
-    seg4_k<<<dim3(8, 1), 512, 0, stream>>>(bufA, bufB, csf, 0);
-    seg5_k<<<dim3(8, 1), 512, 0, stream>>>(bufB, fin, csf, 0);
-    measure_l1<<<1, 1024, 0, stream>>>(fin, out);
+  const size_t need = off;
+
+  float2* csarr = (float2*)(ws + o_cs);
+  float2* csf   = (float2*)(ws + o_csf);
+  float2* lcu   = (float2*)(ws + o_lcu2);
+  float*  pMbuf = (float*)(ws + o_pm);
+  float*  pA    = (float*)(ws + o_pa);
+  float*  parts = (float*)(ws + o_part);
+  unsigned* cnts = (unsigned*)(ws + o_cnt);
+  float2* monoA = (float2*)(ws + o_mA2);
+  float2* monoB = (float2*)(ws + o_mB2);
+  float2* acc   = (float2*)(ws + o_acc2);
+  float2* fin   = (float2*)(ws + o_fin2);
+  float2* bufA  = (float2*)(ws + o_bufA);
+  float2* bufB  = (float2*)(ws + o_bufB);
+
+  angles2_kernel<<<dim3(NPQC, NTOK), 64, 0, stream>>>(emb, W, b, csarr);
+  prep_kernel<<<1, 64, 0, stream>>>(lcuri, lcu, ffp, csf);
+  init3_kernel<<<64, 512, 0, stream>>>(monoA, acc, qsvt, cnts);
+
+  if (ws_size >= need) {
+    mega_k<<<256, 512, 0, stream>>>(csarr, csf, lcu, qsvt,
+                                    monoA, monoB, acc, fin, bufA, bufB,
+                                    pMbuf, pA, parts, out, cnts, cnts + 32);
     return;
   }
 
-  off = 0;
-  const size_t o_ang = nxt(NTOK * NPQC * sizeof(float));
-  const size_t o_lcu = nxt(NTOK * sizeof(float2));
-  const size_t o_nrm = nxt(16 * sizeof(float));
-  const size_t o_mA  = nxt((size_t)DIM * sizeof(float2));
-  const size_t o_mB  = nxt((size_t)DIM * sizeof(float2));
-  const size_t o_acc = nxt((size_t)DIM * sizeof(float2));
-  const size_t o_fin = nxt((size_t)DIM * sizeof(float2));
-  const size_t o_ev  = nxt((size_t)NTOK * DIM * sizeof(float2));
-  const bool bigws = ws_size >= off;
-
-  float*  angles  = (float*)(ws + o_ang);
-  float2* lcu     = (float2*)(ws + o_lcu);
-  float*  norms   = (float*)(ws + o_nrm);
-  float2* monoA   = (float2*)(ws + o_mA);
-  float2* monoB   = (float2*)(ws + o_mB);
-  float2* acc     = (float2*)(ws + o_acc);
-  float2* fin     = (float2*)(ws + o_fin);
-  float2* evolved = (float2*)(ws + o_ev);
-
-  angles_kernel<<<dim3(NPQC, NTOK), 64, 0, stream>>>(emb, W, b, angles);
-  lcu_kernel<<<1, 64, 0, stream>>>(lcuri, lcu);
-  init_kernel<<<DIM / 256, 256, 0, stream>>>(monoA, monoB, acc, qsvt, norms);
-
-  float2* mono = monoA;
-  float2* mono2 = monoB;
+  float2* mIn = monoA;
+  float2* mOut = monoB;
+  const float* prevPM = nullptr;
   for (int k = 1; k <= 3; ++k) {
-    norm_kernel<<<1, 1024, 0, stream>>>(mono, norms, k - 1);
-    if (bigws) {
-      evolve_kernel<<<NTOK, TPB, 0, stream>>>(angles, NPQC, mono, norms, k - 1, 0, lcu, evolved);
-      combine_kernel<<<DIM / 256, 256, 0, stream>>>(evolved, lcu, norms, k - 1, qsvt, k, mono2, acc);
-    } else {
-      evolve_kernel<<<NTOK, TPB, 0, stream>>>(angles, NPQC, mono, norms, k - 1, 2, lcu, mono2);
-      finish_kernel<<<DIM / 256, 256, 0, stream>>>(mono2, acc, mono, norms, k - 1, qsvt, k);
-    }
-    float2* tmp = mono; mono = mono2; mono2 = tmp;
-  }
-
-  norm_kernel<<<1, 1024, 0, stream>>>(acc, norms, 3);
-  evolve_kernel<<<1, TPB, 0, stream>>>(ffp, 0, acc, norms, 3, 1, lcu, fin);
-  measure_kernel<<<1, 1024, 0, stream>>>(fin, out);
-}
+    const int np = prevPM ? 64 : 0;
+    seg1_k<<<dim3(8, NTOK), 512, 0, stream>>>(mIn, bufA, csarr, NPQC, prevPM, np, 0, qsvt);
+    seg2_k<<<dim3(8, NTOK), 512, 0, stream>>>(bufA, bufB, csarr, NPQC);
+    seg3_k<<<dim3(8, NTOK), 512, 0, stream>>>(bufB, bufA, csarr, NPQC);
+    seg4_k<<<dim3(8, NTOK), 512, 0, stream>>>(bufA, bufB, csarr, NPQC);
+    seg5_k<<<dim3(8, NTOK), 512, 0, stream>>>(bufB, bufA, csarr, NPQC);
+    float* pMk = pMbuf + (size_t)(k - 1) * 64;
+    combine2_k<<<64, 512, 0, stream>>>(bufA, lcu, prevPM, np, qsvt, k, mOut, acc, pMk, pA);
+    prevPM = pMk;
+    float2* tmp = mIn; mIn = mOut; mOut = tmp;
+  }
+  seg1_k<<<dim3(8, 1), 512, 0, stream>>>(acc, bufA, csf, 0, pA, 64, 1, qsvt);
+  seg2_k<<<dim3(8, 1), 512, 0, stream>>>(bufA, bufB, csf, 0);
+  seg3_k<<<dim3(8, 1), 512, 0, stream>>>(bufB, bufA, csf, 0);
+  seg4_k<<<dim3(8, 1), 512, 0, stream>>>(bufA, bufB, csf, 0);
+  seg5_k<<<dim3(8, 1), 512, 0, stream>>>(bufB, fin, csf, 0);
+  measure_l1<<<1, 1024, 0, stream>>>(fin, out);
+}
```

Result: slower. 658.5 us (+97.2%).
